# Performance work log

Measured on AMD Instinct MI355X. Metric: run time of the kernel, lower is better.

Reference implementation:

```python
import jax, jax.numpy as jnp
import numpy as np

EMBED_DIM = 1024
NUM_HEADS = 16
HEAD_DIM = EMBED_DIM // NUM_HEADS
SCALE = HEAD_DIM ** -0.5


def setup_inputs() -> dict:
    key = jax.random.key(0)
    k_x, k_wqkv, k_bqkv, k_wp, k_bp = jax.random.split(key, 5)
    B, N = 2, 2048
    x = jax.random.normal(k_x, (B, N, EMBED_DIM), dtype=jnp.float32)
    # torch.nn.Linear default init: U(-1/sqrt(fan_in), 1/sqrt(fan_in))
    lim = 1.0 / np.sqrt(EMBED_DIM)
    W_qkv = jax.random.uniform(k_wqkv, (EMBED_DIM, 3 * EMBED_DIM), jnp.float32, -lim, lim)
    b_qkv = jax.random.uniform(k_bqkv, (3 * EMBED_DIM,), jnp.float32, -lim, lim)
    W_proj = jax.random.uniform(k_wp, (EMBED_DIM, EMBED_DIM), jnp.float32, -lim, lim)
    b_proj = jax.random.uniform(k_bp, (EMBED_DIM,), jnp.float32, -lim, lim)
    return {"x": x, "W_qkv": W_qkv, "b_qkv": b_qkv, "W_proj": W_proj, "b_proj": b_proj}


def reference(x, W_qkv, b_qkv, W_proj, b_proj):
    B, N, C = x.shape
    qkv = x @ W_qkv + b_qkv                              # [B, N, 3C]
    qkv = qkv.reshape(B, N, 3, NUM_HEADS, HEAD_DIM)
    qkv = jnp.transpose(qkv, (2, 0, 3, 1, 4))            # [3, B, H, N, D]
    q, k, v = qkv[0], qkv[1], qkv[2]
    attn = jnp.einsum('bhnd,bhmd->bhnm', q, k) * SCALE   # [B, H, N, N]
    attn = jax.nn.softmax(attn, axis=-1)
    out = jnp.einsum('bhnm,bhmd->bhnd', attn, v)         # [B, H, N, D]
    out = jnp.transpose(out, (0, 2, 1, 3)).reshape(B, N, C)
    return out @ W_proj + b_proj
```

## Files before the change

### kernel.cpp

```cpp
#include <hip/hip_runtime.h>
#include <math.h>

typedef unsigned short u16;
typedef _Float16 f16;
typedef f16 f16x8 __attribute__((ext_vector_type(8)));
typedef __fp16 hp16x2 __attribute__((ext_vector_type(2)));
typedef float f32x4 __attribute__((ext_vector_type(4)));
typedef float f32x16 __attribute__((ext_vector_type(16)));
typedef unsigned u32x2 __attribute__((ext_vector_type(2)));

#define SEQ   2048
#define NH    16
#define HD    64
#define EMB   1024
#define NQKV  3072
#define BATCH 2
#define QSCALE 0.18033688f

__device__ __forceinline__ u16 f2h(float f) {
  union { f16 h; u16 u; } w; w.h = (f16)f; return w.u;
}

__device__ __forceinline__ void gload16(const void* g, void* l) {
  __builtin_amdgcn_global_load_lds(
      (const __attribute__((address_space(1))) unsigned int*)g,
      (__attribute__((address_space(3))) unsigned int*)l, 16, 0, 0);
}

__global__ __launch_bounds__(256) void cvt_x(const float* __restrict__ X,
                                             u16* __restrict__ Xh) {
  const size_t i = ((size_t)blockIdx.x * 256 + threadIdx.x) * 8;
  float4 a = *reinterpret_cast<const float4*>(&X[i]);
  float4 b = *reinterpret_cast<const float4*>(&X[i + 4]);
  union { hp16x2 h2[4]; float4 f; } pk;
  pk.h2[0] = __builtin_amdgcn_cvt_pkrtz(a.x, a.y);
  pk.h2[1] = __builtin_amdgcn_cvt_pkrtz(a.z, a.w);
  pk.h2[2] = __builtin_amdgcn_cvt_pkrtz(b.x, b.y);
  pk.h2[3] = __builtin_amdgcn_cvt_pkrtz(b.z, b.w);
  *reinterpret_cast<float4*>(&Xh[i]) = pk.f;
}

__global__ __launch_bounds__(256) void cvt_wt(const float* __restrict__ W,
                                              u16* __restrict__ Wt,
                                              int K, int N) {
  __shared__ u16 T[64][68];
  const int n0 = blockIdx.x << 6, k0 = blockIdx.y << 6;
  const int t = threadIdx.x;
  const int rr = t >> 4, cc = (t & 15) << 2;
#pragma unroll
  for (int p = 0; p < 4; p++) {
    const int kr = p * 16 + rr;
    float4 v = *reinterpret_cast<const float4*>(&W[(size_t)(k0 + kr) * N + n0 + cc]);
    T[cc + 0][kr] = f2h(v.x); T[cc + 1][kr] = f2h(v.y);
    T[cc + 2][kr] = f2h(v.z); T[cc + 3][kr] = f2h(v.w);
  }
  __syncthreads();
#pragma unroll
  for (int p = 0; p < 4; p++) {
    const int nr = p * 16 + rr;
    union { u16 s[4]; unsigned long long d; } o;
    o.s[0] = T[nr][cc + 0]; o.s[1] = T[nr][cc + 1];
    o.s[2] = T[nr][cc + 2]; o.s[3] = T[nr][cc + 3];
    *reinterpret_cast<unsigned long long*>(&Wt[(size_t)(n0 + nr) * K + k0 + cc]) = o.d;
  }
}

__device__ __forceinline__ void gemm_core(const u16* __restrict__ Ag,
                                          const u16* __restrict__ Bg,
                                          int m0, int n0, int t,
                                          f32x4 acc[4][4]) {
  __shared__ __align__(16) u16 As[128 * 32];
  __shared__ __align__(16) u16 Bs[128 * 32];
  const int lane = t & 63, w = t >> 6;
  const int l15  = lane & 15, quad = lane >> 4;
  const int wm = w >> 1, wn = w & 1;
  const int srow  = lane >> 2;
  const int gslot = (lane & 3) ^ ((srow >> 1) & 3);
  const int xk    = (quad ^ ((l15 >> 1) & 3)) << 3;

  for (int k0 = 0; k0 < EMB; k0 += 32) {
    __syncthreads();
#pragma unroll
    for (int i = 0; i < 2; i++) {
      const int ca = w * 2 + i;
      const int arow = ca * 16 + srow;
      gload16(Ag + (size_t)(m0 + arow) * EMB + k0 + gslot * 8, &As[ca * 512]);
      gload16(Bg + (size_t)(n0 + arow) * EMB + k0 + gslot * 8, &Bs[ca * 512]);
    }
    __syncthreads();
    f16x8 af[4], bf[4];
#pragma unroll
    for (int s = 0; s < 4; s++)
      af[s] = *reinterpret_cast<const f16x8*>(&As[(wm * 64 + s * 16 + l15) * 32 + xk]);
#pragma unroll
    for (int s = 0; s < 4; s++)
      bf[s] = *reinterpret_cast<const f16x8*>(&Bs[(wn * 64 + s * 16 + l15) * 32 + xk]);
#pragma unroll
    for (int i = 0; i < 4; i++)
#pragma unroll
      for (int j = 0; j < 4; j++)
        acc[i][j] = __builtin_amdgcn_mfma_f32_16x16x32_f16(af[i], bf[j], acc[i][j], 0, 0, 0);
  }
}

__global__ __launch_bounds__(256) void k_qkv(const u16* __restrict__ Ag,
                                             const u16* __restrict__ Bg,
                                             const float* __restrict__ bias,
                                             u16* __restrict__ qo,
                                             u16* __restrict__ ko,
                                             u16* __restrict__ vo) {
  const int t = threadIdx.x;
  const int lane = t & 63, w = t >> 6;
  const int l15 = lane & 15, quad = lane >> 4;
  const int wm = w >> 1, wn = w & 1;
  const int m0 = blockIdx.y << 7, n0 = blockIdx.x << 7;
  f32x4 acc[4][4];
#pragma unroll
  for (int i = 0; i < 4; i++)
#pragma unroll
    for (int j = 0; j < 4; j++) acc[i][j] = (f32x4){0.f, 0.f, 0.f, 0.f};
  gemm_core(Ag, Bg, m0, n0, t, acc);
#pragma unroll
  for (int j = 0; j < 4; j++) {
    const int c = n0 + wn * 64 + j * 16 + l15;
    const int which = c >> 10, h = (c >> 6) & 15, d = c & 63;
    const float bv = bias[c];
    const float sc = (which == 0) ? QSCALE : 1.0f;
#pragma unroll
    for (int i = 0; i < 4; i++) {
#pragma unroll
      for (int r = 0; r < 4; r++) {
        const int m  = m0 + wm * 64 + i * 16 + quad * 4 + r;
        const int bb = m >> 11, n = m & (SEQ - 1);
        const u16 val = f2h((acc[i][j][r] + bv) * sc);
        if (which == 2)
          vo[(((size_t)bb * NH + h) * HD + d) * SEQ + n] = val;
        else if (which == 1)
          ko[((((size_t)bb * NH + h) * SEQ) + n) * HD + d] = val;
        else
          qo[((((size_t)bb * NH + h) * SEQ) + n) * HD + d] = val;
      }
    }
  }
}

__global__ __launch_bounds__(256) void k_proj(const u16* __restrict__ Ag,
                                              const u16* __restrict__ Bg,
                                              const float* __restrict__ bias,
                                              float* __restrict__ out) {
  const int t = threadIdx.x;
  const int lane = t & 63, w = t >> 6;
  const int l15 = lane & 15, quad = lane >> 4;
  const int wm = w >> 1, wn = w & 1;
  const int m0 = blockIdx.y << 7, n0 = blockIdx.x << 7;
  f32x4 acc[4][4];
#pragma unroll
  for (int i = 0; i < 4; i++)
#pragma unroll
    for (int j = 0; j < 4; j++) acc[i][j] = (f32x4){0.f, 0.f, 0.f, 0.f};
  gemm_core(Ag, Bg, m0, n0, t, acc);
#pragma unroll
  for (int j = 0; j < 4; j++) {
    const int c = n0 + wn * 64 + j * 16 + l15;
    const float bv = bias[c];
#pragma unroll
    for (int i = 0; i < 4; i++) {
#pragma unroll
      for (int r = 0; r < 4; r++) {
        const int m = m0 + wm * 64 + i * 16 + quad * 4 + r;
        out[(size_t)m * EMB + c] = acc[i][j][r] + bv;
      }
    }
  }
}

__global__ __launch_bounds__(512, 4) void k_attn(const u16* __restrict__ Qg,
                                                 const u16* __restrict__ Kg,
                                                 const u16* __restrict__ Vtg,
                                                 u16* __restrict__ AO) {
  __shared__ __align__(16) u16 KV[2][2][2][64 * 64];
  __shared__ float Lx[256];
  const int t    = threadIdx.x;
  const int lane = t & 63, w = t >> 6;
  const int grp  = w >> 2, wl = w & 3;
  const int l31  = lane & 31, hi = lane >> 5;
  const int id   = blockIdx.y * 16 + blockIdx.x;
  const int swz  = ((id & 7) << 6) | (id >> 3);
  const int bh   = swz >> 4;
  const int q0   = (swz & 15) << 7;
  const size_t base = (size_t)bh * SEQ * HD;

  f16x8 qf[4];
  {
    const u16* qp = Qg + base + (size_t)(q0 + 32 * wl + l31) * HD + hi * 8;
#pragma unroll
    for (int c = 0; c < 4; c++) {
      union { float4 f; f16x8 v; } fu;
      fu.f = *reinterpret_cast<const float4*>(qp + c * 16);
      qf[c] = fu.v;
    }
  }

  f32x16 O0 = {}, O1 = {};
  float lsum = 0.f;
  const int fsw = (l31 >> 1) & 7;
  const int srw = lane >> 3, ssl = lane & 7;
  const int kbeg = grp << 10;
  const int kend = kbeg + (SEQ / 2);

  auto STAGE = [&](int buf, int kt) {
    u16* Ksb = KV[buf][grp][0];
    u16* Vsb = KV[buf][grp][1];
#pragma unroll
    for (int i = 0; i < 2; i++) {
      const int ca  = wl * 2 + i;
      const int row = ca * 8 + srw;
      const int sg  = (ssl ^ ((row >> 1) & 7)) << 3;
      gload16(Kg  + base + (size_t)(kt + row) * HD + sg, &Ksb[ca * 512]);
      gload16(Vtg + base + (size_t)row * SEQ + kt + sg,  &Vsb[ca * 512]);
    }
  };

  STAGE(0, kbeg);
  __syncthreads();

  int cur = 0;
  for (int kt = kbeg; kt < kend; kt += 64) {
    if (kt + 64 < kend) STAGE(cur ^ 1, kt + 64);
    const u16* Ks = KV[cur][grp][0];
    const u16* Vs = KV[cur][grp][1];

#pragma unroll
    for (int sk = 0; sk < 2; sk++) {
      f32x16 c = {};
      __builtin_amdgcn_s_setprio(1);
#pragma unroll
      for (int cc = 0; cc < 4; cc++) {
        f16x8 kf = *reinterpret_cast<const f16x8*>(
            &Ks[(sk * 32 + l31) * 64 + (((cc * 2 + hi) ^ fsw) << 3)]);
        c = __builtin_amdgcn_mfma_f32_32x32x16_f16(kf, qf[cc], c, 0, 0, 0);
      }
      __builtin_amdgcn_s_setprio(0);
      unsigned pw[4][2];
#pragma unroll
      for (int g = 0; g < 4; g++) {
        const float p0 = __builtin_amdgcn_exp2f(c[4 * g + 0]);
        const float p1 = __builtin_amdgcn_exp2f(c[4 * g + 1]);
        const float p2 = __builtin_amdgcn_exp2f(c[4 * g + 2]);
        const float p3 = __builtin_amdgcn_exp2f(c[4 * g + 3]);
        lsum += (p0 + p1) + (p2 + p3);
        union { hp16x2 h; unsigned u; } w0, w1;
        w0.h = __builtin_amdgcn_cvt_pkrtz(p0, p1);
        w1.h = __builtin_amdgcn_cvt_pkrtz(p2, p3);
        pw[g][0] = w0.u; pw[g][1] = w1.u;
      }
      __builtin_amdgcn_s_setprio(1);
#pragma unroll
      for (int s = 0; s < 2; s++) {
        u32x2 r02 = __builtin_amdgcn_permlane32_swap(
            pw[2 * s][0], pw[2 * s + 1][0], false, false);
        u32x2 r13 = __builtin_amdgcn_permlane32_swap(
            pw[2 * s][1], pw[2 * s + 1][1], false, false);
        union { unsigned u[4]; f16x8 v; } fr;
        fr.u[0] = r02.x;
        fr.u[1] = r13.x;
        fr.u[2] = r02.y;
        fr.u[3] = r13.y;
        const int cc = sk * 2 + s;
        f16x8 vf0 = *reinterpret_cast<const f16x8*>(
            &Vs[l31 * 64 + (((cc * 2 + hi) ^ fsw) << 3)]);
        f16x8 vf1 = *reinterpret_cast<const f16x8*>(
            &Vs[(32 + l31) * 64 + (((cc * 2 + hi) ^ fsw) << 3)]);
        O0 = __builtin_amdgcn_mfma_f32_32x32x16_f16(fr.v, vf0, O0, 0, 0, 0);
        O1 = __builtin_amdgcn_mfma_f32_32x32x16_f16(fr.v, vf1, O1, 0, 0, 0);
      }
      __builtin_amdgcn_s_setprio(0);
    }
    __syncthreads();
    cur ^= 1;
  }

  float* Xch = reinterpret_cast<float*>(&KV[0][0][0][0]);
  const int li = wl * 64 + lane;
  if (grp == 1) {
#pragma unroll
    for (int g4 = 0; g4 < 4; g4++) {
      f32x4 v0 = { O0[4 * g4 + 0], O0[4 * g4 + 1], O0[4 * g4 + 2], O0[4 * g4 + 3] };
      *reinterpret_cast<f32x4*>(&Xch[(g4 * 256 + li) * 4]) = v0;
      f32x4 v1 = { O1[4 * g4 + 0], O1[4 * g4 + 1], O1[4 * g4 + 2], O1[4 * g4 + 3] };
      *reinterpret_cast<f32x4*>(&Xch[((4 + g4) * 256 + li) * 4]) = v1;
    }
    Lx[li] = lsum;
  }
  __syncthreads();
  if (grp == 0) {
#pragma unroll
    for (int g4 = 0; g4 < 4; g4++) {
      f32x4 v0 = *reinterpret_cast<const f32x4*>(&Xch[(g4 * 256 + li) * 4]);
      f32x4 v1 = *reinterpret_cast<const f32x4*>(&Xch[((4 + g4) * 256 + li) * 4]);
#pragma unroll
      for (int j = 0; j < 4; j++) {
        O0[4 * g4 + j] += v0[j];
        O1[4 * g4 + j] += v1[j];
      }
    }
    lsum += Lx[li];
    lsum += __shfl_xor(lsum, 32);
    const int b = bh >> 4, h = bh & 15;
#pragma unroll
    for (int g = 0; g < 4; g++) {
#pragma unroll
      for (int rr = 0; rr < 4; rr++) {
        const int r = g * 4 + rr;
        const int qrow = rr + 8 * g + 4 * hi;
        const float inv = 1.f / __shfl(lsum, qrow, 64);
        const int n = q0 + 32 * wl + qrow;
        u16* dst = AO + ((size_t)(b * SEQ + n)) * EMB + h * HD;
        dst[l31]      = f2h(O0[r] * inv);
        dst[32 + l31] = f2h(O1[r] * inv);
      }
    }
  }
}

extern "C" void kernel_launch(void* const* d_in, const int* in_sizes, int n_in,
                              void* d_out, int out_size, void* d_ws, size_t ws_size,
                              hipStream_t stream) {
  (void)in_sizes; (void)n_in; (void)out_size; (void)ws_size;
  const float* x     = (const float*)d_in[0];
  const float* Wqkv  = (const float*)d_in[1];
  const float* bqkv  = (const float*)d_in[2];
  const float* Wproj = (const float*)d_in[3];
  const float* bproj = (const float*)d_in[4];
  float* out = (float*)d_out;

  const size_t NE = (size_t)BATCH * SEQ * EMB;
  u16* q    = (u16*)d_ws;
  u16* k    = q + NE;
  u16* vt   = k + NE;
  u16* aoxh = vt + NE;
  u16* Wt   = aoxh + NE;
  u16* Wpt  = Wt + (size_t)NQKV * EMB;

  cvt_x<<<NE / 2048, 256, 0, stream>>>(x, aoxh);
  dim3 gw1(NQKV / 64, EMB / 64);
  cvt_wt<<<gw1, 256, 0, stream>>>(Wqkv, Wt, EMB, NQKV);
  dim3 gw2(EMB / 64, EMB / 64);
  cvt_wt<<<gw2, 256, 0, stream>>>(Wproj, Wpt, EMB, EMB);

  dim3 gq(NQKV / 128, (BATCH * SEQ) / 128);
  k_qkv<<<gq, 256, 0, stream>>>(aoxh, Wt, bqkv, q, k, vt);

  dim3 ga(SEQ / 128, BATCH * NH);
  k_attn<<<ga, 512, 0, stream>>>(q, k, vt, aoxh);

  dim3 gp(EMB / 128, (BATCH * SEQ) / 128);
  k_proj<<<gp, 256, 0, stream>>>(aoxh, Wpt, bproj, out);
}
```

Measured before the change: 193.7 us.

## Use larger 256x256 QKV GEMM tiles with triple-buffered async LDS pipeline

```diff
diff --git a/kernel.cpp b/kernel.cpp
--- a/kernel.cpp
+++ b/kernel.cpp
@@ -103,36 +103,96 @@
   }
 }
 
-__global__ __launch_bounds__(256) void k_qkv(const u16* __restrict__ Ag,
-                                             const u16* __restrict__ Bg,
-                                             const float* __restrict__ bias,
-                                             u16* __restrict__ qo,
-                                             u16* __restrict__ ko,
-                                             u16* __restrict__ vo) {
+__global__ __launch_bounds__(512, 2) void k_qkv(const u16* __restrict__ Ag,
+                                                const u16* __restrict__ Bg,
+                                                const float* __restrict__ bias,
+                                                u16* __restrict__ qo,
+                                                u16* __restrict__ ko,
+                                                u16* __restrict__ vo) {
+  __shared__ __align__(16) u16 As[3][256 * 32];
+  __shared__ __align__(16) u16 Bs[3][256 * 32];
   const int t = threadIdx.x;
   const int lane = t & 63, w = t >> 6;
   const int l15 = lane & 15, quad = lane >> 4;
-  const int wm = w >> 1, wn = w & 1;
-  const int m0 = blockIdx.y << 7, n0 = blockIdx.x << 7;
-  f32x4 acc[4][4];
-#pragma unroll
-  for (int i = 0; i < 4; i++)
-#pragma unroll
-    for (int j = 0; j < 4; j++) acc[i][j] = (f32x4){0.f, 0.f, 0.f, 0.f};
-  gemm_core(Ag, Bg, m0, n0, t, acc);
-#pragma unroll
-  for (int j = 0; j < 4; j++) {
-    const int c = n0 + wn * 64 + j * 16 + l15;
+  const int wm = w >> 2, wn = w & 3;
+  const int srow  = lane >> 2;
+  const int gslot = (lane & 3) ^ ((srow >> 1) & 3);
+  const int xk    = (quad ^ ((l15 >> 1) & 3)) << 3;
+  const int m0 = blockIdx.y << 8, n0 = blockIdx.x << 8;
+
+  f32x4 acc[8][4];
+#pragma unroll
+  for (int mf = 0; mf < 8; mf++)
+#pragma unroll
+    for (int nf = 0; nf < 4; nf++) acc[mf][nf] = (f32x4){0.f, 0.f, 0.f, 0.f};
+
+  auto STAGE = [&](int buf, int k0) {
+#pragma unroll
+    for (int i = 0; i < 2; i++) {
+      const int ca = w * 2 + i;
+      const int arow = ca * 16 + srow;
+      gload16(Ag + (size_t)(m0 + arow) * EMB + k0 + gslot * 8, &As[buf][ca * 512]);
+      gload16(Bg + (size_t)(n0 + arow) * EMB + k0 + gslot * 8, &Bs[buf][ca * 512]);
+    }
+  };
+
+  STAGE(0, 0);
+  STAGE(1, 32);
+  asm volatile("s_waitcnt vmcnt(4)" ::: "memory");
+  __builtin_amdgcn_sched_barrier(0);
+  __builtin_amdgcn_s_barrier();
+  __builtin_amdgcn_sched_barrier(0);
+
+  int cur = 0, nxt = 2;
+  for (int kt = 0; kt < 32; ++kt) {
+    if (kt + 2 < 32) STAGE(nxt, (kt + 2) * 32);
+
+    f16x8 af[8], bf[4];
+#pragma unroll
+    for (int mf = 0; mf < 8; mf++)
+      af[mf] = *reinterpret_cast<const f16x8*>(
+          &As[cur][(wm * 128 + mf * 16 + l15) * 32 + xk]);
+#pragma unroll
+    for (int nf = 0; nf < 4; nf++)
+      bf[nf] = *reinterpret_cast<const f16x8*>(
+          &Bs[cur][(wn * 64 + nf * 16 + l15) * 32 + xk]);
+
+    __builtin_amdgcn_s_setprio(1);
+#pragma unroll
+    for (int mf = 0; mf < 8; mf++)
+#pragma unroll
+      for (int nf = 0; nf < 4; nf++)
+        acc[mf][nf] = __builtin_amdgcn_mfma_f32_16x16x32_f16(af[mf], bf[nf],
+                                                             acc[mf][nf], 0, 0, 0);
+    __builtin_amdgcn_s_setprio(0);
+
+    asm volatile("s_waitcnt lgkmcnt(0)" ::: "memory");
+    if (kt + 2 < 32) {
+      asm volatile("s_waitcnt vmcnt(4)" ::: "memory");
+    } else {
+      asm volatile("s_waitcnt vmcnt(0)" ::: "memory");
+    }
+    __builtin_amdgcn_sched_barrier(0);
+    __builtin_amdgcn_s_barrier();
+    __builtin_amdgcn_sched_barrier(0);
+
+    cur = (cur == 2) ? 0 : cur + 1;
+    nxt = (nxt == 2) ? 0 : nxt + 1;
+  }
+
+#pragma unroll
+  for (int nf = 0; nf < 4; nf++) {
+    const int c = n0 + wn * 64 + nf * 16 + l15;
     const int which = c >> 10, h = (c >> 6) & 15, d = c & 63;
     const float bv = bias[c];
     const float sc = (which == 0) ? QSCALE : 1.0f;
 #pragma unroll
-    for (int i = 0; i < 4; i++) {
+    for (int mf = 0; mf < 8; mf++) {
 #pragma unroll
       for (int r = 0; r < 4; r++) {
-        const int m  = m0 + wm * 64 + i * 16 + quad * 4 + r;
+        const int m  = m0 + wm * 128 + mf * 16 + quad * 4 + r;
         const int bb = m >> 11, n = m & (SEQ - 1);
-        const u16 val = f2h((acc[i][j][r] + bv) * sc);
+        const u16 val = f2h((acc[mf][nf][r] + bv) * sc);
         if (which == 2)
           vo[(((size_t)bb * NH + h) * HD + d) * SEQ + n] = val;
         else if (which == 1)
@@ -348,8 +408,8 @@
   dim3 gw2(EMB / 64, EMB / 64);
   cvt_wt<<<gw2, 256, 0, stream>>>(Wproj, Wpt, EMB, EMB);
 
-  dim3 gq(NQKV / 128, (BATCH * SEQ) / 128);
-  k_qkv<<<gq, 256, 0, stream>>>(aoxh, Wt, bqkv, q, k, vt);
+  dim3 gq(NQKV / 256, (BATCH * SEQ) / 256);
+  k_qkv<<<gq, 512, 0, stream>>>(aoxh, Wt, bqkv, q, k, vt);
 
   dim3 ga(SEQ / 128, BATCH * NH);
   k_attn<<<ga, 512, 0, stream>>>(q, k, vt, aoxh);
```

Result: slower. 217.9 us (+12.5%).
